# Kernel optimization log

Hardware: AMD Instinct MI355X
Metric: run time of the kernel (lower is better)

Reference implementation:

```python
import jax, jax.numpy as jnp
import numpy as np

D = 1024; NH = 16; HD = D // NH; B = 2; L = 2048
BASE_FAST = (1.0 + 5.0 ** 0.5) / 2.0
BASE_SLOW = 1618.0
BASE_GLU = 16180.0
ALPHA_ATTN = 0.42; ALPHA_MLP = 1.07; ALPHA_ADV = 1.0
H_GATE = max(8, D // 4)   # rope_gate hidden
H_NU = max(4, D // 8)     # DuplexViscosity hidden
LN_EPS = 1e-5


def _rope_cos_sin(seq_len, dim, base, dtype=jnp.float32):
    idx = jnp.arange(0, dim, 2, dtype=dtype) / float(dim)
    inv = 1.0 / (base ** idx)
    t = jnp.arange(seq_len, dtype=dtype)
    freqs = jnp.outer(t, inv)                       # (L, D/2)
    emb = jnp.concatenate([freqs, freqs], axis=-1)  # (L, D)
    return jnp.cos(emb)[None], jnp.sin(emb)[None]   # (1, L, D)


def _rotate_half(x):
    x1, x2 = jnp.split(x, 2, axis=-1)
    return jnp.concatenate([-x2, x1], axis=-1)


def _apply_rope(x, cos, sin):
    return x * cos + _rotate_half(x) * sin


def setup_inputs() -> dict:
    key = jax.random.key(0)
    ks = jax.random.split(key, 16)
    std = 0.02
    # all Linear weights stored as (in, out) so forward is x @ W + b
    return {
        "z": jax.random.normal(ks[0], (B, L, D), jnp.float32),
        "Wq": jax.random.normal(ks[1], (D, D), jnp.float32) * std,
        "bq": jnp.zeros((D,), jnp.float32),
        "Wk": jax.random.normal(ks[2], (D, D), jnp.float32) * std,
        "bk": jnp.zeros((D,), jnp.float32),
        "Wv": jax.random.normal(ks[3], (D, D), jnp.float32) * std,
        "bv": jnp.zeros((D,), jnp.float32),
        "Wcoh": jax.random.normal(ks[4], (D, D), jnp.float32) * std,
        "gamma": jnp.zeros((1,), jnp.float32),
        "rg_w1": jax.random.normal(ks[5], (D, H_GATE), jnp.float32) * std,
        "rg_b1": jnp.zeros((H_GATE,), jnp.float32),
        "rg_w2": jax.random.normal(ks[6], (H_GATE, 1), jnp.float32) * std,
        "rg_b2": jnp.zeros((1,), jnp.float32),
        "nu_diff": jnp.asarray(0.2, jnp.float32),
        "nu_adv": jnp.asarray(0.01, jnp.float32),
        "nu_w1": jax.random.normal(ks[7], (D, H_NU), jnp.float32) * std,
        "nu_b1": jnp.zeros((H_NU,), jnp.float32),
        "nu_w2": jax.random.normal(ks[8], (H_NU, 1), jnp.float32) * std,
        "nu_b2": jnp.zeros((1,), jnp.float32),
        "Wu": jax.random.normal(ks[9], (D, D), jnp.float32) * std,
        "bu": jnp.zeros((D,), jnp.float32),
        "Wg": jax.random.normal(ks[10], (D, D), jnp.float32) * std,
        "bg": jnp.zeros((D,), jnp.float32),
        "ln_w": jnp.ones((D,), jnp.float32),
        "ln_b": jnp.zeros((D,), jnp.float32),
        "Cw": jax.random.normal(ks[11], (D, D), jnp.float32) * std,
        "Cb": jnp.zeros((D,), jnp.float32),
    }


def reference(z, Wq, bq, Wk, bk, Wv, bv, Wcoh, gamma, rg_w1, rg_b1, rg_w2, rg_b2,
              nu_diff, nu_adv, nu_w1, nu_b1, nu_w2, nu_b2, Wu, bu, Wg, bg,
              ln_w, ln_b, Cw, Cb):
    b, l, d = z.shape
    dt = z.dtype
    # causal cumulative mean pool[t] = mean(z[0..t])
    pool = jnp.cumsum(z, axis=1) / jnp.arange(1, l + 1, dtype=dt)[None, :, None]

    # QKV projections
    Q = z @ Wq + bq
    K_raw = z @ Wk + bk
    V = z @ Wv + bv

    # global coherence bias: (B, Lq, Lk)
    gk = pool @ Wcoh
    gb = jnp.einsum('bld,bmd->blm', gk, K_raw) * (d ** -0.5)
    gb = jnp.tanh(gamma[0]) * gb

    # hybrid RoPE gate (small MLP on pool, exact gelu as in torch)
    gate = jax.nn.sigmoid(jax.nn.gelu(pool @ rg_w1 + rg_b1, approximate=False) @ rg_w2 + rg_b2)  # (B,L,1)
    cos_f, sin_f = _rope_cos_sin(l, d, BASE_FAST, dt)
    cos_s, sin_s = _rope_cos_sin(l, d, BASE_SLOW, dt)
    cos = gate * cos_f + (1.0 - gate) * cos_s
    sin = gate * sin_f + (1.0 - gate) * sin_s
    Qr = _apply_rope(Q, cos, sin)
    Kr = _apply_rope(K_raw, cos, sin)

    # multi-head causal attention with fused coherence bias
    Qh = Qr.reshape(b, l, NH, HD).transpose(0, 2, 1, 3)
    Kh = Kr.reshape(b, l, NH, HD).transpose(0, 2, 1, 3)
    Vh = V.reshape(b, l, NH, HD).transpose(0, 2, 1, 3)
    logits = jnp.einsum('bhld,bhmd->bhlm', Qh, Kh) * (HD ** -0.5)
    logits = logits + gb[:, None]
    causal = jnp.tril(jnp.ones((l, l), bool))
    logits = jnp.where(causal[None, None], logits, -jnp.inf)
    attn = jax.nn.softmax(logits, axis=-1)
    attn_out = jnp.einsum('bhlm,bhmd->bhld', attn, Vh).transpose(0, 2, 1, 3).reshape(b, l, d)
    attn_w = attn.mean(axis=1)

    # DuplexViscosity on causal pool
    delta = jnp.tanh(jnp.tanh(pool @ nu_w1 + nu_b1) @ nu_w2 + nu_b2) * jnp.abs(nu_adv)
    nu_b = jnp.abs(nu_diff) + delta  # (B,L,1)

    # GLU branch with fixed slow-base RoPE
    cos_g, sin_g = _rope_cos_sin(l, d, BASE_GLU, dt)
    z_glu = _apply_rope(z, cos_g, sin_g)
    bilinear = (z_glu @ Wu + bu) * (z_glu @ Wg + bg)
    adv = -(ALPHA_ADV * nu_b) * bilinear
    mu = adv.mean(axis=-1, keepdims=True)
    var = ((adv - mu) ** 2).mean(axis=-1, keepdims=True)
    adv_n = (adv - mu) * jax.lax.rsqrt(var + LN_EPS) * ln_w + ln_b
    mlp_out = adv_n @ Cw + Cb

    z_next = z + ALPHA_ATTN * attn_out + ALPHA_MLP * mlp_out
    return z_next, attn_w
```

## Files before the change

### kernel.cpp

```cpp
#include <hip/hip_runtime.h>

#define DD 1024
#define NHH 16
#define HDD 64
#define BB 2
#define LL 2048
#define MM (BB*LL)
#define HG 256
#define HN 128

#define LOG_FAST 0.48121182f
#define LOG_SLOW 7.3889461f
#define LOG_GLU  9.6915312f
#define SCL 0.18033688f

typedef __attribute__((ext_vector_type(8))) short short8;
typedef __attribute__((ext_vector_type(4))) float f32x4;

__device__ __forceinline__ float gelu_f(float x) {
    return 0.5f * x * (1.0f + erff(x * 0.70710678f));
}

__device__ __forceinline__ ushort f2b(float x) {
    unsigned u = __float_as_uint(x);
// ... 281 lines not shown

    f32x4 acc[4][4];
#pragma unroll
    for (int mi = 0; mi < 4; ++mi)
#pragma unroll
        for (int ni = 0; ni < 4; ++ni) acc[mi][ni] = (f32x4){0.f, 0.f, 0.f, 0.f};

    int c0 = wid * 128 + lane;
    int c1 = c0 + 64;
    const ushort* Ag0 = A + (size_t)(m0 + (c0 & 127)) * 1024 + (c0 >> 7) * 8;
    const ushort* Ag1 = A + (size_t)(m0 + (c1 & 127)) * 1024 + (c1 >> 7) * 8;
    const ushort* Bg0 = Wt + (size_t)(n0 + (c0 & 127)) * 1024 + (c0 >> 7) * 8;
    const ushort* Bg1 = Wt + (size_t)(n0 + (c1 & 127)) * 1024 + (c1 >> 7) * 8;
    ushort* Al0 = As + wid * 1024;
    ushort* Al1 = As + wid * 1024 + 512;
    ushort* Bl0 = Bs + wid * 1024;
    ushort* Bl1 = Bs + wid * 1024 + 512;

    const ushort* a_rd = &As[(quad * 128 + wm * 64 + l16) * 8];
    const ushort* b_rd = &Bs[(quad * 128 + wn * 64 + l16) * 8];

    for (int kb = 0; kb < 1024; kb += 32) {
        gl_lds16(Ag0 + kb, Al0);
        gl_lds16(Ag1 + kb, Al1);
        gl_lds16(Bg0 + kb, Bl0);
        gl_lds16(Bg1 + kb, Bl1);
        __syncthreads();
        short8 af[4], bf[4];
#pragma unroll
        for (int mi = 0; mi < 4; ++mi)
            af[mi] = *(const short8*)(a_rd + mi * 16 * 8);
#pragma unroll
        for (int ni = 0; ni < 4; ++ni)
            bf[ni] = *(const short8*)(b_rd + ni * 16 * 8);
#pragma unroll
        for (int mi = 0; mi < 4; ++mi)
#pragma unroll
            for (int ni = 0; ni < 4; ++ni)
                acc[mi][ni] = __builtin_amdgcn_mfma_f32_16x16x32_bf16(
                    af[mi], bf[ni], acc[mi][ni], 0, 0, 0);
        __syncthreads();
    }
#pragma unroll
    for (int mi = 0; mi < 4; ++mi) {
#pragma unroll
        for (int r = 0; r < 4; ++r) {
            int row = m0 + wm * 64 + mi * 16 + quad * 4 + r;
            ushort* Cp = C + (size_t)row * Ndim;
#pragma unroll
            for (int ni = 0; ni < 4; ++ni)
                Cp[n0 + wn * 64 + ni * 16 + l16] = f2b(acc[mi][ni][r]);
        }
    }
}

__global__ __launch_bounds__(256) void gemm_gates(
        const ushort* __restrict__ A, const ushort* __restrict__ WtRG,
        const ushort* __restrict__ WtNU, const float* __restrict__ rg_b1,
        const float* __restrict__ nu_b1, float* __restrict__ H1,
        float* __restrict__ N1) {
    int bx = blockIdx.x;
    bool isH = bx < 2;
    const ushort* Wt = isH ? WtRG : WtNU;
    const float* bias = isH ? rg_b1 : nu_b1;
    float* C = isH ? H1 : N1;
    int Ndim = isH ? HG : HN;
    int n0 = isH ? bx * 128 : 0;
    int m0 = blockIdx.y * 128;
    __shared__ ushort As[4096];
    __shared__ ushort Bs[4096];
    int tid = threadIdx.x;
    int wid = tid >> 6, lane = tid & 63;
    int wm = wid >> 1, wn = wid & 1;
    int quad = lane >> 4, l16 = lane & 15;

    f32x4 acc[4][4];
#pragma unroll
    for (int mi = 0; mi < 4; ++mi)
#pragma unroll
        for (int ni = 0; ni < 4; ++ni) acc[mi][ni] = (f32x4){0.f, 0.f, 0.f, 0.f};

    int c0 = wid * 128 + lane;
    int c1 = c0 + 64;
    const ushort* Ag0 = A + (size_t)(m0 + (c0 & 127)) * 1024 + (c0 >> 7) * 8;
    const ushort* Ag1 = A + (size_t)(m0 + (c1 & 127)) * 1024 + (c1 >> 7) * 8;
    const ushort* Bg0 = Wt + (size_t)(n0 + (c0 & 127)) * 1024 + (c0 >> 7) * 8;
    const ushort* Bg1 = Wt + (size_t)(n0 + (c1 & 127)) * 1024 + (c1 >> 7) * 8;
    ushort* Al0 = As + wid * 1024;
    ushort* Al1 = As + wid * 1024 + 512;
    ushort* Bl0 = Bs + wid * 1024;
    ushort* Bl1 = Bs + wid * 1024 + 512;

    const ushort* a_rd = &As[(quad * 128 + wm * 64 + l16) * 8];
    const ushort* b_rd = &Bs[(quad * 128 + wn * 64 + l16) * 8];

    for (int kb = 0; kb < 1024; kb += 32) {
        gl_lds16(Ag0 + kb, Al0);
        gl_lds16(Ag1 + kb, Al1);
        gl_lds16(Bg0 + kb, Bl0);
        gl_lds16(Bg1 + kb, Bl1);
        __syncthreads();
        short8 af[4], bf[4];
#pragma unroll
        for (int mi = 0; mi < 4; ++mi)
            af[mi] = *(const short8*)(a_rd + mi * 16 * 8);
#pragma unroll
        for (int ni = 0; ni < 4; ++ni)
            bf[ni] = *(const short8*)(b_rd + ni * 16 * 8);
#pragma unroll
        for (int mi = 0; mi < 4; ++mi)
#pragma unroll
            for (int ni = 0; ni < 4; ++ni)
                acc[mi][ni] = __builtin_amdgcn_mfma_f32_16x16x32_bf16(
                    af[mi], bf[ni], acc[mi][ni], 0, 0, 0);
        __syncthreads();
    }
    int bcol[4];
    float bval[4];
#pragma unroll
    for (int ni = 0; ni < 4; ++ni) {
        bcol[ni] = n0 + wn * 64 + ni * 16 + l16;
        bval[ni] = bias[bcol[ni]];
    }
#pragma unroll
    for (int mi = 0; mi < 4; ++mi) {
#pragma unroll
        for (int r = 0; r < 4; ++r) {
            int row = m0 + wm * 64 + mi * 16 + quad * 4 + r;
            float* Cp = C + (size_t)row * Ndim;
#pragma unroll
            for (int ni = 0; ni < 4; ++ni)
                Cp[bcol[ni]] = acc[mi][ni][r] + bval[ni];
        }
    }
}

__global__ __launch_bounds__(256) void gb_mfma(
        const ushort* __restrict__ gk16, const ushort* __restrict__ K16r,
        const float* __restrict__ gamma, ushort* __restrict__ gb) {
    int lt = blockIdx.x >> 4, mt = blockIdx.x & 15;
    if (mt > lt) return;
    int b = blockIdx.y;
    __shared__ ushort As[4096];
    __shared__ ushort Bs[4096];
    int tid = threadIdx.x;
    int wid = tid >> 6, lane = tid & 63;
    int l0 = lt * 128, m0 = mt * 128;
    int wm = wid >> 1, wn = wid & 1;
    int quad = lane >> 4, l16 = lane & 15;

    f32x4 acc[4][4];
#pragma unroll
    for (int mi = 0; mi < 4; ++mi)
#pragma unroll
        for (int ni = 0; ni < 4; ++ni) acc[mi][ni] = (f32x4){0.f, 0.f, 0.f, 0.f};

    int c0 = wid * 128 + lane;
    int c1 = c0 + 64;
    const ushort* Ag0 = gk16 + ((size_t)b * LL + l0 + (c0 & 127)) * 1024 + (c0 >> 7) * 8;
    const ushort* Ag1 = gk16 + ((size_t)b * LL + l0 + (c1 & 127)) * 1024 + (c1 >> 7) * 8;
    const ushort* Bg0 = K16r + ((size_t)b * LL + m0 + (c0 & 127)) * 1024 + (c0 >> 7) * 8;
    const ushort* Bg1 = K16r + ((size_t)b * LL + m0 + (c1 & 127)) * 1024 + (c1 >> 7) * 8;
    ushort* Al0 = As + wid * 1024;
    ushort* Al1 = As + wid * 1024 + 512;
    ushort* Bl0 = Bs + wid * 1024;
    ushort* Bl1 = Bs + wid * 1024 + 512;

    const ushort* a_rd = &As[(quad * 128 + wm * 64 + l16) * 8];
    const ushort* b_rd = &Bs[(quad * 128 + wn * 64 + l16) * 8];

    for (int kb = 0; kb < 1024; kb += 32) {
        gl_lds16(Ag0 + kb, Al0);
        gl_lds16(Ag1 + kb, Al1);
        gl_lds16(Bg0 + kb, Bl0);
        gl_lds16(Bg1 + kb, Bl1);
        __syncthreads();
        short8 af[4], bf[4];
#pragma unroll
        for (int mi = 0; mi < 4; ++mi)
            af[mi] = *(const short8*)(a_rd + mi * 16 * 8);
#pragma unroll
        for (int ni = 0; ni < 4; ++ni)
            bf[ni] = *(const short8*)(b_rd + ni * 16 * 8);
#pragma unroll
        for (int mi = 0; mi < 4; ++mi)
#pragma unroll
            for (int ni = 0; ni < 4; ++ni)
                acc[mi][ni] = __builtin_amdgcn_mfma_f32_16x16x32_bf16(
                    af[mi], bf[ni], acc[mi][ni], 0, 0, 0);
        __syncthreads();
    }
    float scale = tanhf(gamma[0]) * 0.25f;
#pragma unroll
    for (int mi = 0; mi < 4; ++mi) {
#pragma unroll
        for (int r = 0; r < 4; ++r) {
            int row = l0 + wm * 64 + mi * 16 + quad * 4 + r;
            ushort* Cp = gb + ((size_t)b * LL + row) * LL;
            ushort4 o;
            o.x = f2b(acc[mi][0][r] * scale);
            o.y = f2b(acc[mi][1][r] * scale);
            o.z = f2b(acc[mi][2][r] * scale);
            o.w = f2b(acc[mi][3][r] * scale);
            *(ushort4*)(Cp + m0 + wn * 64 + l16 * 4) = o;
        }
    }
}

__global__ __launch_bounds__(256) void gatenu_fin(
        const float* __restrict__ H1, const float* __restrict__ N1,
        const float* __restrict__ rg_w2, const float* __restrict__ rg_b2,
        const float* __restrict__ nu_w2, const float* __restrict__ nu_b2,
        const float* __restrict__ nu_diff, const float* __restrict__ nu_adv,
        float* __restrict__ gate, float* __restrict__ nub) {
    int row = blockIdx.x, tid = threadIdx.x;
    float gv = gelu_f(H1[(size_t)row * HG + tid]) * rg_w2[tid];
    float nv = (tid < HN) ? tanhf(N1[(size_t)row * HN + tid]) * nu_w2[tid] : 0.f;
    for (int off = 32; off; off >>= 1) {
        gv += __shfl_down(gv, off);
        nv += __shfl_down(nv, off);
    }
    __shared__ float pg[4], pn[4];
    if ((tid & 63) == 0) { pg[tid >> 6] = gv; pn[tid >> 6] = nv; }
    __syncthreads();
    if (tid == 0) {
        float ga = pg[0] + pg[1] + pg[2] + pg[3] + rg_b2[0];
        gate[row] = 1.f / (1.f + expf(-ga));
        float na = pn[0] + pn[1] + pn[2] + pn[3] + nu_b2[0];
        nub[row] = fabsf(nu_diff[0]) + tanhf(na) * fabsf(nu_adv[0]);
    }
}

__global__ void rope_qk_bf16(const float* __restrict__ Q, const float* __restrict__ K,
                             const float* __restrict__ gate,
                             ushort* __restrict__ Q16, ushort* __restrict__ K16) {
    int idx = blockIdx.x * 256 + threadIdx.x;
    int row = idx >> 9;
    int i = idx & 511;
    int b = row >> 11, t = row & (LL - 1);
    float g = gate[row];
    float fi = (float)i * (1.0f / 512.0f);
    float tf = (float)t;
    float af = tf * expf(-fi * LOG_FAST);
    float as = tf * expf(-fi * LOG_SLOW);
    float c = g * cosf(af) + (1.f - g) * cosf(as);
    float s = g * sinf(af) + (1.f - g) * sinf(as);
    size_t base = (size_t)row * DD;
    float x = Q[base + i], y = Q[base + 512 + i];
    float q1 = x * c - y * s, q2 = y * c + x * s;
    x = K[base + i]; y = K[base + 512 + i];
    float k1 = x * c - y * s, k2 = y * c + x * s;
    int h1 = i >> 6, d1 = i & 63;
    size_t o1 = ((size_t)(b * 16 + h1) * LL + t) * 64 + d1;
    size_t o2 = ((size_t)(b * 16 + 8 + h1) * LL + t) * 64 + d1;
    Q16[o1] = f2b(q1); Q16[o2] = f2b(q2);
    K16[o1] = f2b(k1); K16[o2] = f2b(k2);
}

__global__ __launch_bounds__(256) void vt16_kernel(const float* __restrict__ V,
                                                   ushort* __restrict__ VT) {
    __shared__ ushort t[64][72];
    int lb = blockIdx.x, hb = blockIdx.y, b = blockIdx.z;
    int tid = threadIdx.x;
    {
        int l = tid >> 2, c0 = (tid & 3) * 16;
        const float* Vp = V + ((size_t)(b * LL) + lb * 64 + l) * DD + hb * 64 + c0;
#pragma unroll
        for (int j = 0; j < 4; ++j) {
            float4 v = *(const float4*)(Vp + j * 4);
            t[l][c0 + j * 4 + 0] = f2b(v.x);
            t[l][c0 + j * 4 + 1] = f2b(v.y);
            t[l][c0 + j * 4 + 2] = f2b(v.z);
            t[l][c0 + j * 4 + 3] = f2b(v.w);
        }
    }
    __syncthreads();
    {
        int d = tid >> 2, l0 = (tid & 3) * 16;
        ushort tmp[16];
#pragma unroll
        for (int j = 0; j < 16; ++j) tmp[j] = t[l0 + j][d];
        ushort* Op = VT + ((size_t)((b * 16 + hb) * 64) + d) * LL + lb * 64 + l0;
        *(ushort4*)(Op + 0)  = *(ushort4*)&tmp[0];
        *(ushort4*)(Op + 4)  = *(ushort4*)&tmp[4];
        *(ushort4*)(Op + 8)  = *(ushort4*)&tmp[8];
        *(ushort4*)(Op + 12) = *(ushort4*)&tmp[12];
    }
}

__global__ void rope_glu_b16(const float* __restrict__ z, ushort* __restrict__ zg) {
    int idx = blockIdx.x * 256 + threadIdx.x;
    int row = idx >> 9;
    int i = idx & 511;
    int t = row & (LL - 1);
    float fi = (float)i * (1.0f / 512.0f);
    float ag = (float)t * expf(-fi * LOG_GLU);
    float c = cosf(ag), s = sinf(ag);
    size_t base = (size_t)row * DD;
    float x = z[base + i], y = z[base + 512 + i];
    zg[base + i]       = f2b(x * c - y * s);
    zg[base + 512 + i] = f2b(y * c + x * s);
}

__global__ __launch_bounds__(256, 2) void attn_flash_mfma(
        const ushort* __restrict__ Q16, const ushort* __restrict__ K16,
        const ushort* __restrict__ VT16, const ushort* __restrict__ gb16,
        float* __restrict__ attn_out, float* __restrict__ stats) {
    int h = blockIdx.x, b = blockIdx.z;
    __shared__ ushort Ks0[4096];
    __shared__ ushort Vs0[4096];
    __shared__ ushort Ks1[4096];
    __shared__ ushort Vs1[4096];
    __shared__ ushort Ps[4096];
    int tid = threadIdx.x, wid = tid >> 6, lane = tid & 63;
    int quad = lane >> 4, l16 = lane & 15;
    const ushort* Qg = Q16 + ((size_t)(b * 16 + h) * LL) * 64;
    const ushort* Kg = K16 + ((size_t)(b * 16 + h) * LL) * 64;
    const ushort* Vg = VT16 + ((size_t)(b * 16 + h) * 64) * LL;
    const ushort* gbB = gb16 + (size_t)b * LL * LL;
    float* stB = stats + ((size_t)(b * 16 + h) * LL) * 2;
    int qrow = wid * 16 + quad * 4;
    ushort* Pw = Ps + wid * 1024;

    short ov = (l16 == 0) ? (short)0x3F80 : (short)0;
    short8 onesf = {ov, ov, ov, ov, ov, ov, ov, ov};

#define FLASH_PHASE(KC, VC, KN, VN, T) do {                                       \
    int k0_ = (T) * 64;                                                           \
    if ((T) + 1 <= qt) {                                                          \
        stage_tile(Kg + (size_t)(k0_ + 64) * 64, 64, (KN), tid);                  \
        stage_tile(Vg + (k0_ + 64), LL, (VN), tid);                               \
    }                                                                             \
    f32x4 sf_[4];                                                                 \
    _Pragma("unroll")                                                             \
    for (int r = 0; r < 4; ++r) {                                                 \
        ushort4 g4_ = *(const ushort4*)(gbB + (size_t)(q0 + qrow + r) * LL + k0_ + l16 * 4); \
        sf_[0][r] = b2f(g4_.x); sf_[1][r] = b2f(g4_.y);                           \
        sf_[2][r] = b2f(g4_.z); sf_[3][r] = b2f(g4_.w);                           \
    }                                                                             \
    _Pragma("unroll")                                                             \
    for (int ks = 0; ks < 2; ++ks)                                                \
        _Pragma("unroll")                                                         \
        for (int nt = 0; nt < 4; ++nt) {                                          \
            short8 kf_ = *(const short8*)((KC) + SWZC(nt * 16 + l16, ks * 4 + quad)); \
            sf_[nt] = __builtin_amdgcn_mfma_f32_16x16x32_bf16(qf[ks], kf_, sf_[nt], 0, 0, 0); \
        }                                                                         \
    if ((T) == qt) {                                                              \
        _Pragma("unroll")                                                         \
        for (int nt = 0; nt < 4; ++nt)                                            \
            _Pragma("unroll")                                                     \
            for (int r = 0; r < 4; ++r)                                           \
                if (nt * 16 + l16 > qrow + r) sf_[nt][r] = -1e30f;                \
    }                                                                             \
    float alpha_[4], mS_[4];                                                      \
    _Pragma("unroll")                                                             \
    for (int r = 0; r < 4; ++r) {                                                 \
        float m_ = fmaxf(fmaxf(sf_[0][r], sf_[1][r]), fmaxf(sf_[2][r], sf_[3][r])); \
        _Pragma("unroll")                                                         \
        for (int off = 1; off < 16; off <<= 1)                                    \
            m_ = fmaxf(m_, __shfl_xor(m_, off));                                  \
        float nm_ = fmaxf(m_r[r], m_);                                            \
        alpha_[r] = __builtin_amdgcn_exp2f((m_r[r] - nm_) * SCL);                 \
        m_r[r] = nm_;                                                             \
        mS_[r] = nm_ * SCL;                                                       \
    }                                                                             \
    _Pragma("unroll")                                                             \
    for (int nt = 0; nt < 4; ++nt)                                                \
        _Pragma("unroll")                                                         \
        for (int r = 0; r < 4; ++r) {                                             \
            float p_ = __builtin_amdgcn_exp2f(fmaf(sf_[nt][r], SCL, -mS_[r]));    \
            int prow_ = quad * 4 + r;                                             \
            int chk_ = (nt * 2) | (l16 >> 3);                                     \
            Pw[prow_ * 64 + ((chk_ ^ (prow_ & 7)) << 3) + (l16 & 7)] = f2b(p_);   \
        }                                                                         \
    _Pragma("unroll")                                                             \
    for (int nt = 0; nt < 5; ++nt)                                                \
        _Pragma("unroll")                                                         \
        for (int r = 0; r < 4; ++r) ofr[nt][r] *= alpha_[r];                      \
    short8 pf_[2];                                                                \
    _Pragma("unroll")                                                             \
    for (int ks = 0; ks < 2; ++ks)                                                \
        pf_[ks] = *(const short8*)(Pw + l16 * 64 + (((ks * 4 + quad) ^ (l16 & 7)) << 3)); \
    __builtin_amdgcn_s_setprio(1);                                                \
    _Pragma("unroll")                                                             \
    for (int ks = 0; ks < 2; ++ks) {                                              \
        _Pragma("unroll")                                                         \
        for (int nt = 0; nt < 4; ++nt) {                                          \
            short8 vf_ = *(const short8*)((VC) + SWZC(nt * 16 + l16, ks * 4 + quad)); \
            ofr[nt] = __builtin_amdgcn_mfma_f32_16x16x32_bf16(pf_[ks], vf_, ofr[nt], 0, 0, 0); \
        }                                                                         \
        ofr[4] = __builtin_amdgcn_mfma_f32_16x16x32_bf16(pf_[ks], onesf, ofr[4], 0, 0, 0); \
    }                                                                             \
    __builtin_amdgcn_s_setprio(0);                                                \
    __syncthreads();                                                              \
} while (0)

#pragma unroll 1
    for (int sel = 0; sel < 2; ++sel) {
        int qt = sel ? (31 - (int)blockIdx.y) : (int)blockIdx.y;
        int q0 = qt * 64;

        short8 qf[2];
        {
            const ushort* qp = Qg + (size_t)(q0 + wid * 16 + l16) * 64 + quad * 8;
            qf[0] = *(const short8*)(qp);
            qf[1] = *(const short8*)(qp + 32);
        }
        stage_tile(Kg, 64, Ks0, tid);
        stage_tile(Vg, LL, Vs0, tid);
        __syncthreads();

        f32x4 ofr[5];
        float m_r[4];
#pragma unroll
        for (int nt = 0; nt < 5; ++nt) ofr[nt] = (f32x4){0.f, 0.f, 0.f, 0.f};
#pragma unroll
        for (int r = 0; r < 4; ++r) m_r[r] = -3e38f;

        for (int kt = 0; kt <= qt; kt += 2) {
            FLASH_PHASE(Ks0, Vs0, Ks1, Vs1, kt);
            if (kt + 1 <= qt) FLASH_PHASE(Ks1, Vs1, Ks0, Vs0, kt + 1);
        }

#pragma unroll
        for (int r = 0; r < 4; ++r) {
            float l = __shfl(ofr[4][r], (lane & 48));
            float rinv = 1.0f / l;
            float* op = attn_out + ((size_t)(b * LL) + q0 + qrow + r) * DD + h * 64 + l16;
#pragma unroll
            for (int nt = 0; nt < 4; ++nt)
                op[nt * 16] = ofr[nt][r] * rinv;
        }
        if (l16 == 0) {
#pragma unroll
            for (int r = 0; r < 4; ++r) {
                size_t si = (size_t)(q0 + qrow + r) * 2;
                stB[si]     = m_r[r];
                stB[si + 1] = ofr[4][r];
            }
        }
    }
#undef FLASH_PHASE
}

__global__ __launch_bounds__(256, 4) void attn_w_mfma(
        const ushort* __restrict__ Q16, const ushort* __restrict__ K16,
        const ushort* __restrict__ gb16, const float* __restrict__ stats,
        float* __restrict__ aw) {
    int qt = blockIdx.x >> 5, kt = blockIdx.x & 31;
    int b = blockIdx.y;
    int tid = threadIdx.x, wid = tid >> 6, lane = tid & 63;
    int quad = lane >> 4, l16 = lane & 15;
    int q0 = qt * 64, k0 = kt * 64;
    int qrow = wid * 16 + quad * 4;
    if (kt > qt) {
        int rr = tid >> 2, c0 = (tid & 3) * 16;
        float4 zv = make_float4(0.f, 0.f, 0.f, 0.f);
        float* p = aw + ((size_t)(b * LL) + q0 + rr) * LL + k0 + c0;
#pragma unroll
        for (int j = 0; j < 4; ++j) *(float4*)(p + j * 4) = zv;
        return;
    }
    __shared__ ushort Qs0[4096];
    __shared__ ushort Ks0[4096];
    __shared__ ushort Qs1[4096];
    __shared__ ushort Ks1[4096];
    float acc[4][4];
#pragma unroll
    for (int nt = 0; nt < 4; ++nt)
#pragma unroll
        for (int r = 0; r < 4; ++r) acc[nt][r] = 0.f;
    f32x4 gacc[4];
    const ushort* gbB = gb16 + (size_t)b * LL * LL;
#pragma unroll
    for (int r = 0; r < 4; ++r) {
        ushort4 g4 = *(const ushort4*)(gbB + (size_t)(q0 + qrow + r) * LL + k0 + l16 * 4);
        gacc[0][r] = b2f(g4.x);
        gacc[1][r] = b2f(g4.y);
        gacc[2][r] = b2f(g4.z);
        gacc[3][r] = b2f(g4.w);
    }
    bool diag = (kt == qt);
    stage_tile(Q16 + ((size_t)(b * 16) * LL + q0) * 64, 64, Qs0, tid);
    stage_tile(K16 + ((size_t)(b * 16) * LL + k0) * 64, 64, Ks0, tid);
    __syncthreads();

#define AW_PHASE(QC, KC, QN, KN, H) do {                                          \
    if ((H) < 15) {                                                               \
        stage_tile(Q16 + ((size_t)(b * 16 + (H) + 1) * LL + q0) * 64, 64, (QN), tid); \
        stage_tile(K16 + ((size_t)(b * 16 + (H) + 1) * LL + k0) * 64, 64, (KN), tid); \
    }                                                                             \
    short8 qf_[2];                                                                \
    _Pragma("unroll")                                                             \
    for (int ks = 0; ks < 2; ++ks)                                                \
        qf_[ks] = *(const short8*)((QC) + SWZC(wid * 16 + l16, ks * 4 + quad));   \
    float mS_[4], li_[4];                                                         \
    {                                                                             \
        const float* sp_ = stats + ((size_t)(b * 16 + (H)) * LL + q0 + qrow) * 2; \
        _Pragma("unroll")                                                         \
        for (int r = 0; r < 4; ++r) {                                             \
            mS_[r] = sp_[r * 2] * SCL;                                            \
            li_[r] = 1.0f / sp_[r * 2 + 1];                                       \
        }                                                                         \
    }                                                                             \
    f32x4 sf_[4];                                                                 \
    _Pragma("unroll")                                                             \
    for (int nt = 0; nt < 4; ++nt) sf_[nt] = gacc[nt];                            \
    __builtin_amdgcn_s_setprio(1);                                                \
    _Pragma("unroll")                                                             \
    for (int ks = 0; ks < 2; ++ks)                                                \
        _Pragma("unroll")                                                         \
        for (int nt = 0; nt < 4; ++nt) {                                          \
            short8 kf_ = *(const short8*)((KC) + SWZC(nt * 16 + l16, ks * 4 + quad)); \
            sf_[nt] = __builtin_amdgcn_mfma_f32_16x16x32_bf16(qf_[ks], kf_, sf_[nt], 0, 0, 0); \
        }                                                                         \
    __builtin_amdgcn_s_setprio(0);                                                \
    _Pragma("unroll")                                                             \
    for (int nt = 0; nt < 4; ++nt)                                                \
        _Pragma("unroll")                                                         \
        for (int r = 0; r < 4; ++r) {                                             \
            int row_ = qrow + r;                                                  \
            if (!diag || (nt * 16 + l16 <= row_))                                 \
                acc[nt][r] += __builtin_amdgcn_exp2f(fmaf(sf_[nt][r], SCL, -mS_[r])) * li_[r]; \
        }                                                                         \
    __syncthreads();                                                              \
} while (0)

    for (int h = 0; h < NHH; h += 2) {
        AW_PHASE(Qs0, Ks0, Qs1, Ks1, h);
        AW_PHASE(Qs1, Ks1, Qs0, Ks0, h + 1);
    }
#undef AW_PHASE

#pragma unroll
    for (int r = 0; r < 4; ++r) {
        float* op = aw + ((size_t)(b * LL) + q0 + qrow + r) * LL + k0 + l16;
#pragma unroll
        for (int nt = 0; nt < 4; ++nt)
            op[nt * 16] = acc[nt][r] * 0.0625f;
    }
}

__global__ __launch_bounds__(256) void adv_ln_kernel(
        const float* __restrict__ U, const float* __restrict__ G,
        const float* __restrict__ nub, const float* __restrict__ lnw,
        const float* __restrict__ lnb, ushort* __restrict__ out) {
    int row = blockIdx.x, tid = threadIdx.x;
    size_t base = (size_t)row * DD + tid * 4;
    float4 u4 = *(const float4*)&U[base];
    float4 g4 = *(const float4*)&G[base];
    float nu = nub[row];
    float a[4];
    a[0] = -nu * u4.x * g4.x;
    a[1] = -nu * u4.y * g4.y;
    a[2] = -nu * u4.z * g4.z;
    a[3] = -nu * u4.w * g4.w;
    float ts = a[0] + a[1] + a[2] + a[3];
    float tq = a[0] * a[0] + a[1] * a[1] + a[2] * a[2] + a[3] * a[3];
    for (int off = 32; off; off >>= 1) {
        ts += __shfl_down(ts, off);
        tq += __shfl_down(tq, off);
    }
    __shared__ float r1[4], r2[4];
    if ((tid & 63) == 0) { r1[tid >> 6] = ts; r2[tid >> 6] = tq; }
    __syncthreads();
    __shared__ float s_mu, s_rs;
    if (tid == 0) {
        float S  = r1[0] + r1[1] + r1[2] + r1[3];
        float Qq = r2[0] + r2[1] + r2[2] + r2[3];
        float mu = S * (1.0f / 1024.f);
        float var = Qq * (1.0f / 1024.f) - mu * mu;
        s_mu = mu;
        s_rs = rsqrtf(var + 1e-5f);
    }
    __syncthreads();
    float mu = s_mu, rs = s_rs;
    float4 w4 = *(const float4*)&lnw[tid * 4];
    float4 b4 = *(const float4*)&lnb[tid * 4];
    ushort4 ov;
    ov.x = f2b((a[0] - mu) * rs * w4.x + b4.x);
    ov.y = f2b((a[1] - mu) * rs * w4.y + b4.y);
    ov.z = f2b((a[2] - mu) * rs * w4.z + b4.z);
    ov.w = f2b((a[3] - mu) * rs * w4.w + b4.w);
    *(ushort4*)&out[base] = ov;
}

__global__ void final_kernel(const float* __restrict__ z, const float* __restrict__ ao,
                             const float* __restrict__ mlp, float* __restrict__ out) {
    size_t i = ((size_t)blockIdx.x * 256 + threadIdx.x) * 4;
    float4 z4 = *(const float4*)&z[i];
    float4 a4 = *(const float4*)&ao[i];
    float4 m4 = *(const float4*)&mlp[i];
    float4 o;
    o.x = z4.x + 0.42f * a4.x + 1.07f * m4.x;
    o.y = z4.y + 0.42f * a4.y + 1.07f * m4.y;
    o.z = z4.z + 0.42f * a4.z + 1.07f * m4.z;
    o.w = z4.w + 0.42f * a4.w + 1.07f * m4.w;
    *(float4*)&out[i] = o;
}

extern "C" void kernel_launch(void* const* d_in, const int* in_sizes, int n_in,
                              void* d_out, int out_size, void* d_ws, size_t ws_size,
                              hipStream_t stream) {
    const float* z       = (const float*)d_in[0];
    const float* Wq      = (const float*)d_in[1];
    const float* bq      = (const float*)d_in[2];
    const float* Wk      = (const float*)d_in[3];
    const float* bk      = (const float*)d_in[4];
    const float* Wv      = (const float*)d_in[5];
    const float* bv      = (const float*)d_in[6];
    const float* Wcoh    = (const float*)d_in[7];
    const float* gamma   = (const float*)d_in[8];
    const float* rg_w1   = (const float*)d_in[9];
    const float* rg_b1   = (const float*)d_in[10];
    const float* rg_w2   = (const float*)d_in[11];
    const float* rg_b2   = (const float*)d_in[12];
    const float* nu_diff = (const float*)d_in[13];
    const float* nu_adv  = (const float*)d_in[14];
    const float* nu_w1   = (const float*)d_in[15];
    const float* nu_b1   = (const float*)d_in[16];
    const float* nu_w2   = (const float*)d_in[17];
    const float* nu_b2   = (const float*)d_in[18];
    const float* Wu      = (const float*)d_in[19];
    const float* bu      = (const float*)d_in[20];
    const float* Wg      = (const float*)d_in[21];
    const float* bg      = (const float*)d_in[22];
    const float* ln_w    = (const float*)d_in[23];
    const float* ln_b    = (const float*)d_in[24];
    const float* Cw      = (const float*)d_in[25];
    const float* Cb      = (const float*)d_in[26];

    float* out_z  = (float*)d_out;
    float* out_aw = out_z + (size_t)MM * DD;

    float* ws = (float*)d_ws;
    const size_t MD = (size_t)MM * DD;
    float* pool  = ws;
    float* Qb    = ws + MD;
    float* Kb    = ws + 2 * MD;
    float* Vb    = ws + 3 * MD;
    float* gkb   = ws + 4 * MD;
    float* gbb   = ws + 5 * MD;
    float* H1    = ws + 7 * MD;
    float* N1    = H1 + (size_t)MM * HG;
    float* gate  = N1 + (size_t)MM * HN;
    float* nub   = gate + MM;
    float* stats = nub + MM;
    float* ctot  = stats + (size_t)BB * NHH * LL * 2;

    char* gbase  = (char*)gbb;
    ushort* Ab   = (ushort*)gbase;
    ushort* Wb   = (ushort*)(gbase + (size_t)8 * 1024 * 1024);
    ushort* gb16 = (ushort*)(gbase + (size_t)16 * 1024 * 1024);
    ushort* WtRG = Wb;
    ushort* WtNU = Wb + (size_t)1024 * 1024;
    ushort* Q16  = (ushort*)Vb;
    ushort* K16  = (ushort*)Vb + MD;
    ushort* VT16 = (ushort*)pool;
    ushort* poolb = (ushort*)pool;
    float*  part = gkb;
    ushort* gk16 = (ushort*)gkb;
    ushort* K16r = (ushort*)gkb + MD;

    dim3 g128(8, 32);
    dim3 wT_g(32, 32);

    pool_scan1<<<dim3(NCH, 4, BB), 256, 0, stream>>>(z, part, ctot, Ab);
    pool_scan2<<<dim3(NCH, 4, BB), 256, 0, stream>>>(part, ctot, poolb);
    f2bT4_kernel<<<dim3(32, 32, 4), 256, 0, stream>>>(Wq, Wk, Wv, Wcoh, Wb);
    gemm_mfma3<<<dim3(8, 32, 3), 256, 0, stream>>>(Ab, Wb, bq, bk, bv, Qb, K16r);
    gemm_mfma_b16out<<<g128, 256, 0, stream>>>(poolb, Wb + (size_t)3 * 1024 * 1024, gk16, DD);
    f2bT_rgnu<<<dim3(8, 32, 2), 256, 0, stream>>>(rg_w1, nu_w1, WtRG, WtNU);
    gemm_gates<<<dim3(3, 32), 256, 0, stream>>>(poolb, WtRG, WtNU, rg_b1, nu_b1, H1, N1);
    gb_mfma<<<dim3(256, BB), 256, 0, stream>>>(gk16, K16r, gamma, gb16);
    gatenu_fin<<<dim3(MM), 256, 0, stream>>>(H1, N1, rg_w2, rg_b2, nu_w2, nu_b2,
                                             nu_diff, nu_adv, gate, nub);
    vt16_kernel<<<dim3(32, 16, BB), 256, 0, stream>>>(Vb, VT16);
    rope_qk_bf16<<<dim3((MM * 512) / 256), 256, 0, stream>>>(Qb, Kb, gate, Q16, K16);
    attn_flash_mfma<<<dim3(NHH, 16, BB), 256, 0, stream>>>(Q16, K16, VT16, gb16, gkb, stats);
    attn_w_mfma<<<dim3(1024, BB), 256, 0, stream>>>(Q16, K16, gb16, stats, out_aw);
    rope_glu_b16<<<dim3((MM * 512) / 256), 256, 0, stream>>>(z, Ab);
    f2bT3_kernel<<<dim3(32, 32, 3), 256, 0, stream>>>(Wu, Wg, Cw, Wb);
    gemm_mfma3<<<dim3(8, 32, 2), 256, 0, stream>>>(Ab, Wb, bu, bg, bg, Qb, nullptr);
    adv_ln_kernel<<<dim3(MM), 256, 0, stream>>>(Qb, Kb, nub, ln_w, ln_b, Ab);
    gemm_mfma<<<g128, 256, 0, stream>>>(Ab, Wb + (size_t)2 * 1024 * 1024, Cb, Qb, DD);
    final_kernel<<<dim3(MD / 4 / 256), 256, 0, stream>>>(z, gkb, Qb, out_z);
}
```

Measured before the change: 565.1 us.

## Triple-buffer flash K/V tiles with vmcnt waits and prefetch bias rows

The flash attention kernel moves from double to triple buffering of K/V tiles in shared memory. Each phase now waits with a partial vmcnt and a raw s_barrier instead of a full __syncthreads, so loads stay in flight across a phase. The gate-bias rows for the next tile are prefetched into registers a phase ahead. The attention-weights kernel likewise issues its stats loads and next-head staging before compute and drops its trailing barriers. Extra LDS use (two more 8KB buffers) may cut occupancy, and the hand-counted vmcnt depends on stage_tile issuing a fixed number of loads.

Result: slower. 586.6 us (+3.8%).

```diff
diff --git a/kernel.cpp b/kernel.cpp
--- a/kernel.cpp
+++ b/kernel.cpp
@@ -616,6 +616,8 @@
     __shared__ ushort Vs0[4096];
     __shared__ ushort Ks1[4096];
     __shared__ ushort Vs1[4096];
+    __shared__ ushort Ks2[4096];
+    __shared__ ushort Vs2[4096];
     __shared__ ushort Ps[4096];
     int tid = threadIdx.x, wid = tid >> 6, lane = tid & 63;
     int quad = lane >> 4, l16 = lane & 15;
@@ -630,18 +632,28 @@
     short ov = (l16 == 0) ? (short)0x3F80 : (short)0;
     short8 onesf = {ov, ov, ov, ov, ov, ov, ov, ov};
 
-#define FLASH_PHASE(KC, VC, KN, VN, T) do {                                       \
-    int k0_ = (T) * 64;                                                           \
-    if ((T) + 1 <= qt) {                                                          \
-        stage_tile(Kg + (size_t)(k0_ + 64) * 64, 64, (KN), tid);                  \
-        stage_tile(Vg + (k0_ + 64), LL, (VN), tid);                               \
+#define FLASH_PHASE(KC, VC, KS, VS, T) do {                                       \
+    asm volatile("s_waitcnt vmcnt(8)" ::: "memory");                              \
+    __builtin_amdgcn_sched_barrier(0);                                            \
+    __builtin_amdgcn_s_barrier();                                                 \
+    __builtin_amdgcn_sched_barrier(0);                                            \
+    {                                                                             \
+        int tg_ = ((T) + 1 <= qt) ? ((T) + 1) : qt;                               \
+        const ushort* gp_ = gbB + (size_t)(q0 + qrow) * LL + tg_ * 64 + l16 * 4;  \
+        gnx[0] = *(const ushort4*)(gp_);                                          \
+        gnx[1] = *(const ushort4*)(gp_ + LL);                                     \
+        gnx[2] = *(const ushort4*)(gp_ + 2 * LL);                                 \
+        gnx[3] = *(const ushort4*)(gp_ + 3 * LL);                                 \
+        int ts_ = ((T) + 2 <= qt) ? ((T) + 2) : qt;                               \
+        stage_tile(Kg + (size_t)ts_ * 64 * 64, 64, (KS), tid);                    \
+        stage_tile(Vg + ts_ * 64, LL, (VS), tid);                                 \
     }                                                                             \
+    __builtin_amdgcn_sched_barrier(0);                                            \
     f32x4 sf_[4];                                                                 \
     _Pragma("unroll")                                                             \
     for (int r = 0; r < 4; ++r) {                                                 \
-        ushort4 g4_ = *(const ushort4*)(gbB + (size_t)(q0 + qrow + r) * LL + k0_ + l16 * 4); \
-        sf_[0][r] = b2f(g4_.x); sf_[1][r] = b2f(g4_.y);                           \
-        sf_[2][r] = b2f(g4_.z); sf_[3][r] = b2f(g4_.w);                           \
+        sf_[0][r] = b2f(gcur[r].x); sf_[1][r] = b2f(gcur[r].y);                   \
+        sf_[2][r] = b2f(gcur[r].z); sf_[3][r] = b2f(gcur[r].w);                   \
     }                                                                             \
     _Pragma("unroll")                                                             \
     for (int ks = 0; ks < 2; ++ks)                                                \
@@ -697,13 +709,18 @@
         ofr[4] = __builtin_amdgcn_mfma_f32_16x16x32_bf16(pf_[ks], onesf, ofr[4], 0, 0, 0); \
     }                                                                             \
     __builtin_amdgcn_s_setprio(0);                                                \
-    __syncthreads();                                                              \
+    gcur[0] = gnx[0]; gcur[1] = gnx[1]; gcur[2] = gnx[2]; gcur[3] = gnx[3];       \
 } while (0)
 
 #pragma unroll 1
     for (int sel = 0; sel < 2; ++sel) {
         int qt = sel ? (31 - (int)blockIdx.y) : (int)blockIdx.y;
         int q0 = qt * 64;
+
+        asm volatile("s_waitcnt vmcnt(0)" ::: "memory");
+        __builtin_amdgcn_sched_barrier(0);
+        __builtin_amdgcn_s_barrier();
+        __builtin_amdgcn_sched_barrier(0);
 
         short8 qf[2];
         {
@@ -713,7 +730,19 @@
         }
         stage_tile(Kg, 64, Ks0, tid);
         stage_tile(Vg, LL, Vs0, tid);
-        __syncthreads();
+        ushort4 gcur[4], gnx[4];
+        {
+            const ushort* gp = gbB + (size_t)(q0 + qrow) * LL + l16 * 4;
+            gcur[0] = *(const ushort4*)(gp);
+            gcur[1] = *(const ushort4*)(gp + LL);
+            gcur[2] = *(const ushort4*)(gp + 2 * LL);
+            gcur[3] = *(const ushort4*)(gp + 3 * LL);
+        }
+        {
+            int t1 = (qt >= 1) ? 1 : 0;
+            stage_tile(Kg + (size_t)t1 * 64 * 64, 64, Ks1, tid);
+            stage_tile(Vg + t1 * 64, LL, Vs1, tid);
+        }
 
         f32x4 ofr[5];
         float m_r[4];
@@ -722,9 +751,10 @@
 #pragma unroll
         for (int r = 0; r < 4; ++r) m_r[r] = -3e38f;
 
-        for (int kt = 0; kt <= qt; kt += 2) {
-            FLASH_PHASE(Ks0, Vs0, Ks1, Vs1, kt);
+        for (int kt = 0; kt <= qt; kt += 3) {
+            FLASH_PHASE(Ks0, Vs0, Ks2, Vs2, kt);
             if (kt + 1 <= qt) FLASH_PHASE(Ks1, Vs1, Ks0, Vs0, kt + 1);
+            if (kt + 2 <= qt) FLASH_PHASE(Ks2, Vs2, Ks1, Vs1, kt + 2);
         }
 
 #pragma unroll
@@ -788,26 +818,29 @@
     bool diag = (kt == qt);
     stage_tile(Q16 + ((size_t)(b * 16) * LL + q0) * 64, 64, Qs0, tid);
     stage_tile(K16 + ((size_t)(b * 16) * LL + k0) * 64, 64, Ks0, tid);
-    __syncthreads();
 
 #define AW_PHASE(QC, KC, QN, KN, H) do {                                          \
-    if ((H) < 15) {                                                               \
-        stage_tile(Q16 + ((size_t)(b * 16 + (H) + 1) * LL + q0) * 64, 64, (QN), tid); \
-        stage_tile(K16 + ((size_t)(b * 16 + (H) + 1) * LL + k0) * 64, 64, (KN), tid); \
-    }                                                                             \
-    short8 qf_[2];                                                                \
-    _Pragma("unroll")                                                             \
-    for (int ks = 0; ks < 2; ++ks)                                                \
-        qf_[ks] = *(const short8*)((QC) + SWZC(wid * 16 + l16, ks * 4 + quad));   \
-    float mS_[4], li_[4];                                                         \
+    asm volatile("s_waitcnt vmcnt(0)" ::: "memory");                              \
+    __builtin_amdgcn_sched_barrier(0);                                            \
+    __builtin_amdgcn_s_barrier();                                                 \
+    __builtin_amdgcn_sched_barrier(0);                                            \
+    float s0_[4], s1_[4];                                                         \
     {                                                                             \
         const float* sp_ = stats + ((size_t)(b * 16 + (H)) * LL + q0 + qrow) * 2; \
         _Pragma("unroll")                                                         \
-        for (int r = 0; r < 4; ++r) {                                             \
-            mS_[r] = sp_[r * 2] * SCL;                                            \
-            li_[r] = 1.0f / sp_[r * 2 + 1];                                       \
-        }                                                                         \
+        for (int r = 0; r < 4; ++r) { s0_[r] = sp_[r * 2]; s1_[r] = sp_[r * 2 + 1]; } \
     }                                                                             \
+    __builtin_amdgcn_sched_barrier(0);                                            \
+    {                                                                             \
+        int hn_ = ((H) + 1 <= 15) ? ((H) + 1) : 15;                               \
+        stage_tile(Q16 + ((size_t)(b * 16 + hn_) * LL + q0) * 64, 64, (QN), tid); \
+        stage_tile(K16 + ((size_t)(b * 16 + hn_) * LL + k0) * 64, 64, (KN), tid); \
+    }                                                                             \
+    __builtin_amdgcn_sched_barrier(0);                                            \
+    short8 qf_[2];                                                                \
+    _Pragma("unroll")                                                             \
+    for (int ks = 0; ks < 2; ++ks)                                                \
+        qf_[ks] = *(const short8*)((QC) + SWZC(wid * 16 + l16, ks * 4 + quad));   \
     f32x4 sf_[4];                                                                 \
     _Pragma("unroll")                                                             \
     for (int nt = 0; nt < 4; ++nt) sf_[nt] = gacc[nt];                            \
@@ -820,6 +853,9 @@
             sf_[nt] = __builtin_amdgcn_mfma_f32_16x16x32_bf16(qf_[ks], kf_, sf_[nt], 0, 0, 0); \
         }                                                                         \
     __builtin_amdgcn_s_setprio(0);                                                \
+    float mS_[4], li_[4];                                                         \
+    _Pragma("unroll")                                                             \
+    for (int r = 0; r < 4; ++r) { mS_[r] = s0_[r] * SCL; li_[r] = 1.0f / s1_[r]; } \
     _Pragma("unroll")                                                             \
     for (int nt = 0; nt < 4; ++nt)                                                \
         _Pragma("unroll")                                                         \
@@ -828,7 +864,6 @@
             if (!diag || (nt * 16 + l16 <= row_))                                 \
                 acc[nt][r] += __builtin_amdgcn_exp2f(fmaf(sf_[nt][r], SCL, -mS_[r])) * li_[r]; \
         }                                                                         \
-    __syncthreads();                                                              \
 } while (0)
 
     for (int h = 0; h < NHH; h += 2) {
```

## Split flash attention into one block per query tile with prefetched bias and barriers

Applied to the files above, without the earlier changes.

The flash attention kernel now launches one block per (head, query tile, batch), with a hashed query-tile order, instead of pairing light and heavy causal tiles inside one block. The gb bias tile for the next key block is prefetched into registers alongside the K/V staging, and the per-phase trailing syncthreads is replaced by a vmcnt wait plus barrier at the start of each phase. Occupancy is raised to 4 blocks per CU. The intent is to hide global-load latency and improve scheduling across CUs. The cost is the loss of the paired load balancing, which can leave uneven tail work, plus higher register pressure from the prefetch buffers.

New measurement: 594.3 us. 1.05x slower.

```diff
diff --git a/kernel.cpp b/kernel.cpp
--- a/kernel.cpp
+++ b/kernel.cpp
@@ -607,11 +607,16 @@
     zg[base + 512 + i] = f2b(y * c + x * s);
 }
 
-__global__ __launch_bounds__(256, 2) void attn_flash_mfma(
+__global__ __launch_bounds__(256, 4) void attn_flash_mfma(
         const ushort* __restrict__ Q16, const ushort* __restrict__ K16,
         const ushort* __restrict__ VT16, const ushort* __restrict__ gb16,
         float* __restrict__ attn_out, float* __restrict__ stats) {
-    int h = blockIdx.x, b = blockIdx.z;
+    int x = blockIdx.x;
+    int b = blockIdx.y;
+    int h = x >> 5;
+    int yidx = x & 31;
+    int qt = (yidx + h * 5 + b * 11) & 31;
+    int q0 = qt * 64;
     __shared__ ushort Ks0[4096];
     __shared__ ushort Vs0[4096];
     __shared__ ushort Ks1[4096];
@@ -630,18 +635,51 @@
     short ov = (l16 == 0) ? (short)0x3F80 : (short)0;
     short8 onesf = {ov, ov, ov, ov, ov, ov, ov, ov};
 
-#define FLASH_PHASE(KC, VC, KN, VN, T) do {                                       \
-    int k0_ = (T) * 64;                                                           \
-    if ((T) + 1 <= qt) {                                                          \
-        stage_tile(Kg + (size_t)(k0_ + 64) * 64, 64, (KN), tid);                  \
-        stage_tile(Vg + (k0_ + 64), LL, (VN), tid);                               \
+    short8 qf[2];
+    {
+        const ushort* qp = Qg + (size_t)(q0 + wid * 16 + l16) * 64 + quad * 8;
+        qf[0] = *(const short8*)(qp);
+        qf[1] = *(const short8*)(qp + 32);
+    }
+    stage_tile(Kg, 64, Ks0, tid);
+    stage_tile(Vg, LL, Vs0, tid);
+    ushort4 gcur[4], gnx[4];
+    {
+        const ushort* gp = gbB + (size_t)(q0 + qrow) * LL + l16 * 4;
+        gcur[0] = *(const ushort4*)(gp);
+        gcur[1] = *(const ushort4*)(gp + LL);
+        gcur[2] = *(const ushort4*)(gp + 2 * LL);
+        gcur[3] = *(const ushort4*)(gp + 3 * LL);
+    }
+
+    f32x4 ofr[5];
+    float m_r[4];
+#pragma unroll
+    for (int nt = 0; nt < 5; ++nt) ofr[nt] = (f32x4){0.f, 0.f, 0.f, 0.f};
+#pragma unroll
+    for (int r = 0; r < 4; ++r) m_r[r] = -3e38f;
+
+#define FLASH_PHASE(KC, VC, KS, VS, T) do {                                       \
+    asm volatile("s_waitcnt vmcnt(0)" ::: "memory");                              \
+    __builtin_amdgcn_sched_barrier(0);                                            \
+    __builtin_amdgcn_s_barrier();                                                 \
+    __builtin_amdgcn_sched_barrier(0);                                            \
+    {                                                                             \
+        int tg_ = ((T) + 1 <= qt) ? ((T) + 1) : qt;                               \
+        const ushort* gp_ = gbB + (size_t)(q0 + qrow) * LL + tg_ * 64 + l16 * 4;  \
+        gnx[0] = *(const ushort4*)(gp_);                                          \
+        gnx[1] = *(const ushort4*)(gp_ + LL);                                     \
+        gnx[2] = *(const ushort4*)(gp_ + 2 * LL);                                 \
+        gnx[3] = *(const ushort4*)(gp_ + 3 * LL);                                 \
+        stage_tile(Kg + (size_t)tg_ * 64 * 64, 64, (KS), tid);                    \
+        stage_tile(Vg + tg_ * 64, LL, (VS), tid);                                 \
     }                                                                             \
+    __builtin_amdgcn_sched_barrier(0);                                            \
     f32x4 sf_[4];                                                                 \
     _Pragma("unroll")                                                             \
     for (int r = 0; r < 4; ++r) {                                                 \
-        ushort4 g4_ = *(const ushort4*)(gbB + (size_t)(q0 + qrow + r) * LL + k0_ + l16 * 4); \
-        sf_[0][r] = b2f(g4_.x); sf_[1][r] = b2f(g4_.y);                           \
-        sf_[2][r] = b2f(g4_.z); sf_[3][r] = b2f(g4_.w);                           \
+        sf_[0][r] = b2f(gcur[r].x); sf_[1][r] = b2f(gcur[r].y);                   \
+        sf_[2][r] = b2f(gcur[r].z); sf_[3][r] = b2f(gcur[r].w);                   \
     }                                                                             \
     _Pragma("unroll")                                                             \
     for (int ks = 0; ks < 2; ++ks)                                                \
@@ -697,55 +735,32 @@
         ofr[4] = __builtin_amdgcn_mfma_f32_16x16x32_bf16(pf_[ks], onesf, ofr[4], 0, 0, 0); \
     }                                                                             \
     __builtin_amdgcn_s_setprio(0);                                                \
-    __syncthreads();                                                              \
+    gcur[0] = gnx[0]; gcur[1] = gnx[1]; gcur[2] = gnx[2]; gcur[3] = gnx[3];       \
 } while (0)
 
-#pragma unroll 1
-    for (int sel = 0; sel < 2; ++sel) {
-        int qt = sel ? (31 - (int)blockIdx.y) : (int)blockIdx.y;
-        int q0 = qt * 64;
-
-        short8 qf[2];
-        {
-            const ushort* qp = Qg + (size_t)(q0 + wid * 16 + l16) * 64 + quad * 8;
-            qf[0] = *(const short8*)(qp);
-            qf[1] = *(const short8*)(qp + 32);
+    for (int kt = 0; kt <= qt; kt += 2) {
+        FLASH_PHASE(Ks0, Vs0, Ks1, Vs1, kt);
+        if (kt + 1 <= qt) FLASH_PHASE(Ks1, Vs1, Ks0, Vs0, kt + 1);
+    }
+#undef FLASH_PHASE
+
+#pragma unroll
+    for (int r = 0; r < 4; ++r) {
+        float l = __shfl(ofr[4][r], (lane & 48));
+        float rinv = 1.0f / l;
+        float* op = attn_out + ((size_t)(b * LL) + q0 + qrow + r) * DD + h * 64 + l16;
+#pragma unroll
+        for (int nt = 0; nt < 4; ++nt)
+            op[nt * 16] = ofr[nt][r] * rinv;
+    }
+    if (l16 == 0) {
+#pragma unroll
+        for (int r = 0; r < 4; ++r) {
+            size_t si = (size_t)(q0 + qrow + r) * 2;
+            stB[si]     = m_r[r];
+            stB[si + 1] = ofr[4][r];
         }
-        stage_tile(Kg, 64, Ks0, tid);
-        stage_tile(Vg, LL, Vs0, tid);
-        __syncthreads();
-
-        f32x4 ofr[5];
-        float m_r[4];
-#pragma unroll
-        for (int nt = 0; nt < 5; ++nt) ofr[nt] = (f32x4){0.f, 0.f, 0.f, 0.f};
-#pragma unroll
-        for (int r = 0; r < 4; ++r) m_r[r] = -3e38f;
-
-        for (int kt = 0; kt <= qt; kt += 2) {
-            FLASH_PHASE(Ks0, Vs0, Ks1, Vs1, kt);
-            if (kt + 1 <= qt) FLASH_PHASE(Ks1, Vs1, Ks0, Vs0, kt + 1);
-        }
-
-#pragma unroll
-        for (int r = 0; r < 4; ++r) {
-            float l = __shfl(ofr[4][r], (lane & 48));
-            float rinv = 1.0f / l;
-            float* op = attn_out + ((size_t)(b * LL) + q0 + qrow + r) * DD + h * 64 + l16;
-#pragma unroll
-            for (int nt = 0; nt < 4; ++nt)
-                op[nt * 16] = ofr[nt][r] * rinv;
-        }
-        if (l16 == 0) {
-#pragma unroll
-            for (int r = 0; r < 4; ++r) {
-                size_t si = (size_t)(q0 + qrow + r) * 2;
-                stB[si]     = m_r[r];
-                stB[si + 1] = ofr[4][r];
-            }
-        }
-    }
-#undef FLASH_PHASE
+    }
 }
 
 __global__ __launch_bounds__(256, 4) void attn_w_mfma(
@@ -982,7 +997,7 @@
                                              nu_diff, nu_adv, gate, nub);
     vt16_kernel<<<dim3(32, 16, BB), 256, 0, stream>>>(Vb, VT16);
     rope_qk_bf16<<<dim3((MM * 512) / 256), 256, 0, stream>>>(Qb, Kb, gate, Q16, K16);
-    attn_flash_mfma<<<dim3(NHH, 16, BB), 256, 0, stream>>>(Q16, K16, VT16, gb16, gkb, stats);
+    attn_flash_mfma<<<dim3(512, BB), 256, 0, stream>>>(Q16, K16, VT16, gb16, gkb, stats);
     attn_w_mfma<<<dim3(1024, BB), 256, 0, stream>>>(Q16, K16, gb16, stats, out_aw);
     rope_glu_b16<<<dim3((MM * 512) / 256), 256, 0, stream>>>(z, Ab);
     f2bT3_kernel<<<dim3(32, 32, 3), 256, 0, stream>>>(Wu, Wg, Cw, Wb);
```
